# Optimization experiments

Measured on AMD Instinct MI355X. Metric: run time of the kernel, lower is better.

The kernel has to match this reference:

```python
import jax, jax.numpy as jnp
import numpy as np
from jax import lax

EPS = 1e-5
T, N, E = 10, 10000, 320000
C_IN, C_HID, C_OUT = 16, 32, 16


def _stgcn_layer(x, edge_index, edge_weight, tw, tb, gw, gb, gamma, beta):
    # x: [T, N, Cin] -> temporal conv over T per node
    xc = jnp.transpose(x, (1, 2, 0))  # [N, Cin, T]
    y = lax.conv_general_dilated(xc, tw, window_strides=(1,), padding=((1, 1),),
                                 dimension_numbers=("NCH", "OIH", "NCH"))
    y = y + tb[None, :, None]
    y = jnp.clip(y, -10.0, 10.0)
    # InstanceNorm1d (affine, biased var over time axis)
    mu = jnp.mean(y, axis=-1, keepdims=True)
    var = jnp.mean((y - mu) ** 2, axis=-1, keepdims=True)
    y = (y - mu) * lax.rsqrt(var + EPS) * gamma[None, :, None] + beta[None, :, None]
    y = jax.nn.relu(y)
    h = jnp.transpose(y, (0, 2, 1))  # [N, T, C]

    n = h.shape[0]
    # GCNConv normalization (identical at every timestep -> computed once)
    ewn = jax.nn.softmax(edge_weight)  # softmax over all E edges
    loop = jnp.arange(n, dtype=edge_index.dtype)
    row = jnp.concatenate([edge_index[0], loop])  # sources (+self loops)
    col = jnp.concatenate([edge_index[1], loop])  # destinations
    w = jnp.concatenate([ewn, jnp.ones((n,), dtype=ewn.dtype)])
    deg = jax.ops.segment_sum(w, col, num_segments=n)
    dinv = jnp.where(deg > 0, lax.rsqrt(jnp.maximum(deg, EPS * 0 + 1e-30)), 0.0)
    norm = dinv[row] * w * dinv[col]  # [E+N]

    hw = jnp.einsum("ntc,cd->ntd", h, gw)  # [N, T, C]
    msg = hw[row] * norm[:, None, None]     # [E+N, T, C] gather
    agg = jax.ops.segment_sum(msg, col, num_segments=n) + gb  # scatter-add
    out = jnp.clip(jax.nn.relu(agg), -10.0, 10.0)
    return jnp.transpose(out, (1, 0, 2))  # [T, N, C]


def setup_inputs() -> dict:
    key = jax.random.key(0)
    ks = jax.random.split(key, 16)
    inp = {
        "x": jax.random.normal(ks[0], (T, N, C_IN), dtype=jnp.float32),
        "edge_index": jax.random.randint(ks[1], (2, E), 0, N, dtype=jnp.int32),
        "edge_weight": jax.random.uniform(ks[2], (E,), dtype=jnp.float32),
        # layer 1 (in -> hid)
        "l1_tw": jax.random.normal(ks[3], (C_HID, C_IN, 3), dtype=jnp.float32) * 0.02,
        "l1_tb": jnp.zeros((C_HID,), dtype=jnp.float32),
        "l1_gw": jax.random.normal(ks[4], (C_HID, C_HID), dtype=jnp.float32) * 0.1,
        "l1_gb": jnp.zeros((C_HID,), dtype=jnp.float32),
        "l1_gamma": jnp.ones((C_HID,), dtype=jnp.float32),
        "l1_beta": jnp.zeros((C_HID,), dtype=jnp.float32),
        # layer 2 (hid -> hid)
        "l2_tw": jax.random.normal(ks[5], (C_HID, C_HID, 3), dtype=jnp.float32) * 0.02,
        "l2_tb": jnp.zeros((C_HID,), dtype=jnp.float32),
        "l2_gw": jax.random.normal(ks[6], (C_HID, C_HID), dtype=jnp.float32) * 0.1,
        "l2_gb": jnp.zeros((C_HID,), dtype=jnp.float32),
        "l2_gamma": jnp.ones((C_HID,), dtype=jnp.float32),
        "l2_beta": jnp.zeros((C_HID,), dtype=jnp.float32),
        # output linear
        "out_w": jax.random.normal(ks[7], (C_HID, C_OUT), dtype=jnp.float32) * 0.1,
        "out_b": jnp.zeros((C_OUT,), dtype=jnp.float32),
    }
    return inp


def reference(x, edge_index, edge_weight,
              l1_tw, l1_tb, l1_gw, l1_gb, l1_gamma, l1_beta,
              l2_tw, l2_tb, l2_gw, l2_gb, l2_gamma, l2_beta,
              out_w, out_b):
    h = _stgcn_layer(x, edge_index, edge_weight, l1_tw, l1_tb, l1_gw, l1_gb, l1_gamma, l1_beta)
    h = _stgcn_layer(h, edge_index, edge_weight, l2_tw, l2_tb, l2_gw, l2_gb, l2_gamma, l2_beta)
    # per-timestep linear then mean over time == mean then linear, done faithfully
    outs = jnp.einsum("tnc,cd->tnd", h, out_w) + out_b
    return jnp.mean(outs, axis=0)  # [N, C_OUT]
```

## Files before the change

### kernel.cpp

```cpp
#include <hip/hip_runtime.h>
#include <hip/hip_bf16.h>
#include <string.h>


typedef __hip_bfloat16 bf16;

#define TSTEPS 10
#define TPAD 12
#define CHID 32
#define ROWELE (TSTEPS * CHID)
#define ROWW4 40

__device__ __forceinline__ float b2f(bf16 v) { return __bfloat162float(v); }
__device__ __forceinline__ float ldf(const void* p, long i, int bf) {
    return bf ? __bfloat162float(((const bf16*)p)[i]) : ((const float*)p)[i];
}
__device__ __forceinline__ int detect_bf(const unsigned* gbits) {
    return (gbits[0] != 0x3F800000u) ? 1 : 0;
}
__device__ __forceinline__ float bflo(unsigned u) { return __uint_as_float(u << 16); }
__device__ __forceinline__ float bfhi(unsigned u) { return __uint_as_float(u & 0xFFFF0000u); }
__device__ __forceinline__ unsigned pack2bf(float a, float b) {
    bf16 x = __float2bfloat16(a), y = __float2bfloat16(b);
    unsigned short ux, uy;
    memcpy(&ux, &x, 2); memcpy(&uy, &y, 2);
    return (unsigned)ux | ((unsigned)uy << 16);
}
__device__ __forceinline__ unsigned short bfbits(float a) {
    bf16 x = __float2bfloat16(a);
    unsigned short u; memcpy(&u, &x, 2);
    return u;
}
__device__ __forceinline__ void accum8(float* f, uint4 u, float w) {
    f[0] += w * bflo(u.x); f[1] += w * bfhi(u.x);
    f[2] += w * bflo(u.y); f[3] += w * bfhi(u.y);
    f[4] += w * bflo(u.z); f[5] += w * bfhi(u.z);
    f[6] += w * bflo(u.w); f[7] += w * bfhi(u.w);
}


__device__ __forceinline__ void edge_body(
    int bb, const void* __restrict__ ew, int bf, const int* __restrict__ ei,
    float* __restrict__ ewn, float* __restrict__ degx, int* __restrict__ cnt,
    float* __restrict__ sumexp, int E, int tid) {
    __shared__ float s_red[4];
    int i0 = (bb * 256 + tid) * 4;
    float e0 = 0.0f, e1 = 0.0f, e2 = 0.0f, e3 = 0.0f;
    if ((E & 3) == 0 && i0 + 3 < E) {
        float w0, w1, w2, w3;
        if (bf) {
            uint2 u = ((const uint2*)ew)[i0 >> 2];
            w0 = bflo(u.x); w1 = bfhi(u.x); w2 = bflo(u.y); w3 = bfhi(u.y);
        } else {
            float4 f = ((const float4*)ew)[i0 >> 2];
            w0 = f.x; w1 = f.y; w2 = f.z; w3 = f.w;
        }
        e0 = __expf(w0); e1 = __expf(w1); e2 = __expf(w2); e3 = __expf(w3);
        int4 c4 = *(const int4*)&ei[E + i0];
        atomicAdd(&degx[c4.x], e0); atomicAdd(&cnt[c4.x], 1);
        atomicAdd(&degx[c4.y], e1); atomicAdd(&cnt[c4.y], 1);
        atomicAdd(&degx[c4.z], e2); atomicAdd(&cnt[c4.z], 1);
        atomicAdd(&degx[c4.w], e3); atomicAdd(&cnt[c4.w], 1);
        *(float4*)&ewn[i0] = make_float4(e0, e1, e2, e3);
    } else {
        float es[4] = {0, 0, 0, 0};
        for (int j = 0; j < 4; j++) {
            int i = i0 + j;
            if (i < E) {
                float e = __expf(ldf(ew, i, bf));
                es[j] = e;
                ewn[i] = e;
                int c = ei[E + i];
                atomicAdd(&degx[c], e);
                atomicAdd(&cnt[c], 1);
            }
        }
        e0 = es[0]; e1 = es[1]; e2 = es[2]; e3 = es[3];
    }
    float v = (e0 + e1) + (e2 + e3);
    for (int o = 32; o > 0; o >>= 1) v += __shfl_down(v, o);
    int lane = tid & 63, wv = tid >> 6;
    if (lane == 0) s_red[wv] = v;
    __syncthreads();
    if (tid == 0) atomicAdd(sumexp, s_red[0] + s_red[1] + s_red[2] + s_red[3]);
}


template <int CIN, int LAYOUT>
__device__ __forceinline__ void conv_body(
    int bb, const void* __restrict__ in_, int bfw,
    const void* __restrict__ tw, const void* __restrict__ tb,
    const void* __restrict__ gamma, const void* __restrict__ beta,
    const void* __restrict__ gw,
    bf16* __restrict__ hw, int N, int tid) {
    constexpr int CO = CHID;
    __shared__ __align__(16) float s_in[8 * CIN * TPAD];
    __shared__ __align__(16) float s_h[8 * CO * TPAD];
    __shared__ __align__(16) unsigned s_tw01[CIN * CO];
    __shared__ __align__(16) unsigned short s_tw2[CIN * CO];
    __shared__ __align__(16) unsigned s_gwp[(CO / 2) * CO];

    int nl = tid >> 5, o = tid & 31;

    float tbv = ldf(tb, o, bfw);
    float gav = ldf(gamma, o, bfw);
    float bev = ldf(beta, o, bfw);

    for (int i = tid; i < CIN * CO; i += 256) {
        int ci = i / CO, oo = i % CO;
        long base = ((long)oo * CIN + ci) * 3;
        float w0 = ldf(tw, base, bfw);
        float w1 = ldf(tw, base + 1, bfw);
        float w2 = ldf(tw, base + 2, bfw);
        s_tw01[ci * CO + oo] = pack2bf(w0, w1);
        s_tw2[ci * CO + oo] = bfbits(w2);
    }
    for (int i = tid; i < (CO / 2) * CO; i += 256) {
        int cp = i / CO, oo = i % CO;
        s_gwp[i] = pack2bf(ldf(gw, (long)(2 * cp) * CO + oo, bfw),
                           ldf(gw, (long)(2 * cp + 1) * CO + oo, bfw));
    }

    int nb = bb * 8;

    if (LAYOUT == 0) {
        constexpr int CP = CIN / 2;
        for (int i2 = tid; i2 < 8 * TSTEPS * CP; i2 += 256) {
            int cp = i2 % CP;
            int t = (i2 / CP) % TSTEPS;
            int nn = i2 / (CP * TSTEPS);
            int n = nb + nn;
            float v0 = 0.0f, v1 = 0.0f;
            if (n < N) {
                long idx = (long)t * ((long)N * CIN) + (long)n * CIN + 2 * cp;
                if (bfw) {
                    unsigned u = ((const unsigned*)in_)[idx >> 1];
                    v0 = bflo(u); v1 = bfhi(u);
                } else {
                    float2 f = ((const float2*)in_)[idx >> 1];
                    v0 = f.x; v1 = f.y;
                }
            }
            int b = nn * (CIN * TPAD) + (2 * cp) * TPAD + t;
            s_in[b] = v0;
            s_in[b + TPAD] = v1;
        }
    } else {
        for (int i2 = tid; i2 < 8 * CIN * 5; i2 += 256) {
            int tp = i2 % 5;
            int ci = (i2 / 5) % CIN;
            int nn = i2 / (5 * CIN);
            int n = nb + nn;
            float v0 = 0.0f, v1 = 0.0f;
            if (n < N) {
                long idx = (long)n * (CIN * TSTEPS) + ci * TSTEPS + 2 * tp;
                unsigned u = ((const unsigned*)in_)[idx >> 1];
                v0 = bflo(u); v1 = bfhi(u);
            }
            int b = nn * (CIN * TPAD) + ci * TPAD + 2 * tp;
            s_in[b] = v0;
            s_in[b + 1] = v1;
        }
    }
    __syncthreads();

    int n = nb + nl;
    const float* xrow = &s_in[nl * CIN * TPAD];

    float acc[TSTEPS];
#pragma unroll
    for (int t = 0; t < TSTEPS; t++) acc[t] = tbv;

    for (int ci = 0; ci < CIN; ci++) {
        const float4* xp = (const float4*)&xrow[ci * TPAD];
        float4 A = xp[0], B = xp[1], C = xp[2];
        float xr[TSTEPS] = {A.x, A.y, A.z, A.w, B.x, B.y, B.z, B.w, C.x, C.y};
        unsigned w01 = s_tw01[ci * CO + o];
        float w0 = bflo(w01), w1 = bfhi(w01);
        float w2 = __uint_as_float(((unsigned)s_tw2[ci * CO + o]) << 16);
        acc[0] += xr[0] * w1 + xr[1] * w2;
#pragma unroll
        for (int t = 1; t < TSTEPS - 1; t++)
            acc[t] += xr[t - 1] * w0 + xr[t] * w1 + xr[t + 1] * w2;
        acc[TSTEPS - 1] += xr[TSTEPS - 2] * w0 + xr[TSTEPS - 1] * w1;
    }

#pragma unroll
    for (int t = 0; t < TSTEPS; t++) acc[t] = fminf(fmaxf(acc[t], -10.0f), 10.0f);
    float mu = 0.0f;
#pragma unroll
    for (int t = 0; t < TSTEPS; t++) mu += acc[t];
    mu *= 0.1f;
    float var = 0.0f;
#pragma unroll
    for (int t = 0; t < TSTEPS; t++) { float d = acc[t] - mu; var += d * d; }
    var *= 0.1f;
    float sc = gav * rsqrtf(var + 1e-5f);
    float h[TSTEPS];
#pragma unroll
    for (int t = 0; t < TSTEPS; t++) h[t] = fmaxf((acc[t] - mu) * sc + bev, 0.0f);

    float4* hp = (float4*)&s_h[nl * CO * TPAD + o * TPAD];
    hp[0] = make_float4(h[0], h[1], h[2], h[3]);
    hp[1] = make_float4(h[4], h[5], h[6], h[7]);
    hp[2] = make_float4(h[8], h[9], 0.0f, 0.0f);
    __syncthreads();

    float acc2[TSTEPS];
#pragma unroll
    for (int t = 0; t < TSTEPS; t++) acc2[t] = 0.0f;
    const float* hrow = &s_h[nl * CO * TPAD];
    for (int cp = 0; cp < CO / 2; cp++) {
        unsigned g2 = s_gwp[cp * CO + o];
        float g0 = bflo(g2), g1 = bfhi(g2);
        const float4* r0 = (const float4*)&hrow[(2 * cp) * TPAD];
        const float4* r1 = (const float4*)&hrow[(2 * cp + 1) * TPAD];
        float4 A0 = r0[0], B0 = r0[1], C0 = r0[2];
        float4 A1 = r1[0], B1 = r1[1], C1 = r1[2];
        acc2[0] += A0.x * g0 + A1.x * g1;
        acc2[1] += A0.y * g0 + A1.y * g1;
        acc2[2] += A0.z * g0 + A1.z * g1;
        acc2[3] += A0.w * g0 + A1.w * g1;
        acc2[4] += B0.x * g0 + B1.x * g1;
        acc2[5] += B0.y * g0 + B1.y * g1;
        acc2[6] += B0.z * g0 + B1.z * g1;
        acc2[7] += B0.w * g0 + B1.w * g1;
        acc2[8] += C0.x * g0 + C1.x * g1;
        acc2[9] += C0.y * g0 + C1.y * g1;
    }
    if (n < N) {
        unsigned* hwp = (unsigned*)hw;
        long base = (long)n * (ROWELE / 2) + o * (TSTEPS / 2);
#pragma unroll
        for (int j = 0; j < 5; j++)
            hwp[base + j] = pack2bf(acc2[2 * j], acc2[2 * j + 1]);
    }
}


__global__ __launch_bounds__(256) void edge_conv1_kernel(
    const void* __restrict__ ew, const unsigned* __restrict__ gbits,
    const int* __restrict__ ei,
    float* __restrict__ ewn, float* __restrict__ degx, int* __restrict__ cnt,
    float* __restrict__ sumexp, int E, int gE4,
    const void* __restrict__ x,
    const void* __restrict__ tw, const void* __restrict__ tb,
    const void* __restrict__ gamma, const void* __restrict__ beta,
    const void* __restrict__ gw,
    bf16* __restrict__ hw, int N) {
    int bf = detect_bf(gbits);
    int tid = threadIdx.x;
    if ((int)blockIdx.x < gE4) {
        edge_body(blockIdx.x, ew, bf, ei, ewn, degx, cnt, sumexp, E, tid);
    } else {
        conv_body<16, 0>(blockIdx.x - gE4, x, bf, tw, tb, gamma, beta, gw,
                         hw, N, tid);
    }
}

__global__ __launch_bounds__(256) void conv2_kernel(
    const void* __restrict__ in_, const unsigned* __restrict__ gbits,
    const void* __restrict__ tw, const void* __restrict__ tb,
    const void* __restrict__ gamma, const void* __restrict__ beta,
    const void* __restrict__ gw,
    bf16* __restrict__ hw, int N) {
    conv_body<32, 1>(blockIdx.x, in_, detect_bf(gbits), tw, tb, gamma, beta,
                     gw, hw, N, threadIdx.x);
}

__global__ __launch_bounds__(1024) void scan_kernel(const int* __restrict__ cnt,
                                                    const float* __restrict__ degx,
                                                    const float* __restrict__ sumexp,
                                                    float* __restrict__ dinv,
                                                    int* __restrict__ off, int N) {
    __shared__ int s[1024];
    int tid = threadIdx.x;
    float invS = 1.0f / (*sumexp);
    for (int i = tid; i < N; i += 1024) dinv[i] = rsqrtf(1.0f + degx[i] * invS);
    int chunk = (N + 1023) / 1024;
    int b0 = tid * chunk;
    int p = 0;
    for (int k = 0; k < chunk; k++) { int i = b0 + k; if (i < N) p += cnt[i]; }
    s[tid] = p;
    __syncthreads();
    for (int d = 1; d < 1024; d <<= 1) {
        int v = (tid >= d) ? s[tid - d] : 0;
        __syncthreads();
        s[tid] += v;
        __syncthreads();
    }
    int base = s[tid] - p;
    for (int k = 0; k < chunk; k++) {
        int i = b0 + k;
        if (i < N) {
            off[i] = base;
            base += cnt[i];
            if (i == N - 1) off[N] = base;
        }
    }
}


__global__ __launch_bounds__(256) void fill_kernel(const int* __restrict__ ei,
                                                   const float* __restrict__ ewn,
                                                   const float* __restrict__ dinv,
                                                   const float* __restrict__ sumexp,
                                                   const int* __restrict__ off,
                                                   int* __restrict__ cursor,
                                                   int2* __restrict__ csr, int E) {
    int i0 = (blockIdx.x * 256 + threadIdx.x) * 4;
    if (i0 >= E) return;
    float invS = 1.0f / (*sumexp);
    if ((E & 3) == 0 && i0 + 3 < E) {
        int4 r4 = *(const int4*)&ei[i0];
        int4 c4 = *(const int4*)&ei[E + i0];
        float4 e4 = *(const float4*)&ewn[i0];
        int rr[4] = {r4.x, r4.y, r4.z, r4.w};
        int cc[4] = {c4.x, c4.y, c4.z, c4.w};
        float ee[4] = {e4.x, e4.y, e4.z, e4.w};
#pragma unroll
        for (int j = 0; j < 4; j++) {
            int r = rr[j], c = cc[j];
            int p = atomicAdd(&cursor[c], 1);
            float w = dinv[r] * (ee[j] * invS) * dinv[c];
            csr[off[c] + p] = make_int2(r, __float_as_int(w));
        }
    } else {
        for (int j = 0; j < 4; j++) {
            int i = i0 + j;
            if (i >= E) break;
            int r = ei[i], c = ei[E + i];
            int p = atomicAdd(&cursor[c], 1);
            float w = dinv[r] * (ewn[i] * invS) * dinv[c];
            csr[off[c] + p] = make_int2(r, __float_as_int(w));
        }
    }
}


template <bool FINAL>
__global__ __launch_bounds__(320) void agg_kernel_t(
    const uint4* __restrict__ hw4, const int* __restrict__ off,
    const int2* __restrict__ csr,
    const float* __restrict__ dinv, const void* __restrict__ gb,
    const void* __restrict__ ow, const void* __restrict__ ob,
    const unsigned* __restrict__ gbits,
    void* __restrict__ out, int N) {
    __shared__ int2 s_sw[ROWELE];
    __shared__ float s_part[8 * ROWW4 * 9];
    __shared__ float s_hbar[CHID];
    __shared__ float s_ow[CHID * 16];
    __shared__ float s_ob[16];

    int bf = detect_bf(gbits);
    int n = blockIdx.x;
    int tid = threadIdx.x;
    int g = tid % ROWW4;
    int eo = tid / ROWW4;

    if (FINAL) {
        for (int i = tid; i < CHID * 16; i += ROWELE) s_ow[i] = ldf(ow, i, bf);
        if (tid < 16) s_ob[tid] = ldf(ob, tid, bf);
    }

    float facc[8];
#pragma unroll
    for (int j = 0; j < 8; j++) facc[j] = 0.0f;

    float dn = dinv[n];
    if (eo == 0) {
        uint4 u = hw4[n * ROWW4 + g];
        accum8(facc, u, dn * dn);
    }

    int beg = off[n], end = off[n + 1];
    for (int base = beg; base < end; base += ROWELE) {
        int m = min(ROWELE, end - base);
        if (tid < m) s_sw[tid] = csr[base + tid];
        __syncthreads();
        int kmax = (m + 7) >> 3;
        int k = 0;
        for (; k + 2 <= kmax; k += 2) {
            int j0 = (k << 3) + eo, j1 = j0 + 8;
            int c0 = min(j0, m - 1), c1 = min(j1, m - 1);
            int2 e0 = s_sw[c0], e1 = s_sw[c1];
            float w0 = (j0 < m) ? __int_as_float(e0.y) : 0.0f;
            float w1 = (j1 < m) ? __int_as_float(e1.y) : 0.0f;
            uint4 u0 = hw4[e0.x * ROWW4 + g];
            uint4 u1 = hw4[e1.x * ROWW4 + g];
            accum8(facc, u0, w0);
            accum8(facc, u1, w1);
        }
        if (k < kmax) {
            int j0 = (k << 3) + eo;
            int c0 = min(j0, m - 1);
            int2 e0 = s_sw[c0];
            float w0 = (j0 < m) ? __int_as_float(e0.y) : 0.0f;
            uint4 u0 = hw4[e0.x * ROWW4 + g];
            accum8(facc, u0, w0);
        }
        __syncthreads();
    }

    {
        float* rowp = &s_part[(eo * ROWW4 + g) * 9];
#pragma unroll
        for (int j = 0; j < 8; j++) rowp[j] = facc[j];
    }
    __syncthreads();
    int gg = tid >> 3, jj = tid & 7;
    float v = 0.0f;
#pragma unroll
    for (int s = 0; s < 8; s++) v += s_part[(s * ROWW4 + gg) * 9 + jj];
    int c = tid / TSTEPS;
    v += ldf(gb, c, bf);
    v = fminf(fmaxf(v, 0.0f), 10.0f);

    if (!FINAL) {
        ((bf16*)out)[(long)n * ROWELE + tid] = __float2bfloat16(v);
    } else {
        __syncthreads();
        s_part[tid] = v;
        __syncthreads();
        if (tid < CHID) {
            float s = 0.0f;
#pragma unroll
            for (int t = 0; t < TSTEPS; t++) s += s_part[tid * TSTEPS + t];
            s_hbar[tid] = s * 0.1f;
        }
        __syncthreads();
        if (tid < 16) {
            float a = s_ob[tid];
#pragma unroll
            for (int cc = 0; cc < CHID; cc++) a += s_hbar[cc] * s_ow[cc * 16 + tid];
            long oi = (long)n * 16 + tid;
            if (bf) ((bf16*)out)[oi] = __float2bfloat16(a);
            else    ((float*)out)[oi] = a;
        }
    }
}


extern "C" void kernel_launch(void* const* d_in, const int* in_sizes, int n_in,
                              void* d_out, int out_size, void* d_ws, size_t ws_size,
                              hipStream_t stream) {
    (void)n_in; (void)out_size; (void)ws_size;

    const void* x     = d_in[0];
    const int*  ei    = (const int*)d_in[1];
    const void* ew    = d_in[2];
    const void* l1_tw = d_in[3];
    const void* l1_tb = d_in[4];
    const void* l1_gw = d_in[5];
    const void* l1_gb = d_in[6];
    const unsigned* gbits = (const unsigned*)d_in[7];
    const void* l1_ga = d_in[7];
    const void* l1_be = d_in[8];
    const void* l2_tw = d_in[9];
    const void* l2_tb = d_in[10];
    const void* l2_gw = d_in[11];
    const void* l2_gb = d_in[12];
    const void* l2_ga = d_in[13];
    const void* l2_be = d_in[14];
    const void* out_w = d_in[15];
    const void* out_b = d_in[16];

    int N = in_sizes[0] / (TSTEPS * 16);
    int E = in_sizes[1] / 2;

    char* p = (char*)d_ws;
    auto alloc = [&](size_t bytes) -> char* {
        char* r = p;
        p += (bytes + 255) & ~(size_t)255;
        return r;
    };
    char* zbase   = p;
    float* sumexp = (float*)alloc(256);
    float* degx   = (float*)alloc((size_t)N * 4);
    int*   cnt    = (int*)alloc((size_t)N * 4);
    int*   cursor = (int*)alloc((size_t)N * 4);
    size_t zbytes = (size_t)(p - zbase);
    float* ewn     = (float*)alloc((size_t)E * 4);
    float* dinv    = (float*)alloc((size_t)N * 4);
    int*   offA    = (int*)alloc((size_t)(N + 1) * 4);
    int2*  csr     = (int2*)alloc((size_t)E * 8);
    bf16*  bufA    = (bf16*)alloc((size_t)N * ROWELE * 2);
    bf16*  bufB    = (bf16*)alloc((size_t)N * ROWELE * 2);

    int gE4 = (E + 1023) / 1024;
    int gConv = (N + 7) / 8;

    hipMemsetAsync(zbase, 0, zbytes, stream);
    hipLaunchKernelGGL(edge_conv1_kernel, dim3(gE4 + gConv), dim3(256), 0, stream,
                       ew, gbits, ei, ewn, degx, cnt, sumexp, E, gE4,
                       x, l1_tw, l1_tb, l1_ga, l1_be, l1_gw, bufA, N);
    hipLaunchKernelGGL(scan_kernel, dim3(1), dim3(1024), 0, stream,
                       cnt, degx, sumexp, dinv, offA, N);
    hipLaunchKernelGGL(fill_kernel, dim3(gE4), dim3(256), 0, stream,
                       ei, ewn, dinv, sumexp, offA, cursor, csr, E);

    hipLaunchKernelGGL((agg_kernel_t<false>), dim3(N), dim3(ROWELE), 0, stream,
                       (const uint4*)bufA, offA, csr, dinv, l1_gb,
                       nullptr, nullptr, gbits, (void*)bufB, N);
    hipLaunchKernelGGL(conv2_kernel, dim3(gConv), dim3(256), 0, stream,
                       (const void*)bufB, gbits, l2_tw, l2_tb, l2_ga, l2_be,
                       l2_gw, bufA, N);
    hipLaunchKernelGGL((agg_kernel_t<true>), dim3(N), dim3(ROWELE), 0, stream,
                       (const uint4*)bufA, offA, csr, dinv, l2_gb,
                       out_w, out_b, gbits, d_out, N);
}
```

Baseline: 278.6 us.

## Split conv work across time pairs with 640-thread blocks of four nodes

Rewrites the temporal conv plus GCN linear body so each thread computes two timesteps of one output channel for one node, using 640-thread blocks that cover four nodes, instead of one thread per (node, channel) computing all ten timesteps. Instance-norm statistics are now computed through shared memory with extra barriers, and the edge softmax/degree pass is resized to the 640-thread block. The goal is more parallelism and lower per-thread register pressure in the conv kernels. In exchange it adds more synchronisation and shared-memory traffic, and the weight-staging cost is amortised over fewer nodes per block.

```diff
diff --git a/kernel.cpp b/kernel.cpp
--- a/kernel.cpp
+++ b/kernel.cpp
@@ -6,12 +6,12 @@
 typedef __hip_bfloat16 bf16;
 
 #define TSTEPS 10
-#define TPAD 12
 #define CHID 32
 #define ROWELE (TSTEPS * CHID)
 #define ROWW4 40
-
-__device__ __forceinline__ float b2f(bf16 v) { return __bfloat162float(v); }
+#define NB 4
+#define CTH 640
+
 __device__ __forceinline__ float ldf(const void* p, long i, int bf) {
     return bf ? __bfloat162float(((const bf16*)p)[i]) : ((const float*)p)[i];
 }
@@ -43,8 +43,8 @@
     int bb, const void* __restrict__ ew, int bf, const int* __restrict__ ei,
     float* __restrict__ ewn, float* __restrict__ degx, int* __restrict__ cnt,
     float* __restrict__ sumexp, int E, int tid) {
-    __shared__ float s_red[4];
-    int i0 = (bb * 256 + tid) * 4;
+    __shared__ float s_red[CTH / 64];
+    int i0 = (bb * CTH + tid) * 4;
     float e0 = 0.0f, e1 = 0.0f, e2 = 0.0f, e3 = 0.0f;
     if ((E & 3) == 0 && i0 + 3 < E) {
         float w0, w1, w2, w3;
@@ -82,57 +82,62 @@
     int lane = tid & 63, wv = tid >> 6;
     if (lane == 0) s_red[wv] = v;
     __syncthreads();
-    if (tid == 0) atomicAdd(sumexp, s_red[0] + s_red[1] + s_red[2] + s_red[3]);
+    if (tid == 0) {
+        float s = 0.0f;
+#pragma unroll
+        for (int w = 0; w < CTH / 64; w++) s += s_red[w];
+        atomicAdd(sumexp, s);
+    }
 }
 
 
 template <int CIN, int LAYOUT>
-__device__ __forceinline__ void conv_body(
+__device__ __forceinline__ void conv_body_tp(
     int bb, const void* __restrict__ in_, int bfw,
     const void* __restrict__ tw, const void* __restrict__ tb,
     const void* __restrict__ gamma, const void* __restrict__ beta,
     const void* __restrict__ gw,
-    bf16* __restrict__ hw, int N, int tid) {
+    unsigned* __restrict__ hw, int N, int tid) {
     constexpr int CO = CHID;
-    __shared__ __align__(16) float s_in[8 * CIN * TPAD];
-    __shared__ __align__(16) float s_h[8 * CO * TPAD];
-    __shared__ __align__(16) unsigned s_tw01[CIN * CO];
-    __shared__ __align__(16) unsigned short s_tw2[CIN * CO];
-    __shared__ __align__(16) unsigned s_gwp[(CO / 2) * CO];
-
-    int nl = tid >> 5, o = tid & 31;
+    __shared__ float s_x[NB * CIN * TSTEPS];
+    __shared__ float s_y[NB * CO * TSTEPS];
+    __shared__ float s_hh[NB * CO * TSTEPS];
+    __shared__ unsigned s_tw01[CIN * CO];
+    __shared__ unsigned short s_tw2[CIN * CO];
+    __shared__ unsigned s_gwp[(CO / 2) * CO];
+    __shared__ float s_mu[NB * CO], s_sc[NB * CO];
+
+    int nl = tid / 160;
+    int rem = tid % 160;
+    int o = rem / 5, j = rem % 5, t0 = 2 * j;
+    int nb = bb * NB;
+    int n = nb + nl;
 
     float tbv = ldf(tb, o, bfw);
-    float gav = ldf(gamma, o, bfw);
     float bev = ldf(beta, o, bfw);
 
-    for (int i = tid; i < CIN * CO; i += 256) {
-        int ci = i / CO, oo = i % CO;
+    for (int i = tid; i < CIN * CO; i += CTH) {
+        int ci = i >> 5, oo = i & 31;
         long base = ((long)oo * CIN + ci) * 3;
-        float w0 = ldf(tw, base, bfw);
-        float w1 = ldf(tw, base + 1, bfw);
-        float w2 = ldf(tw, base + 2, bfw);
-        s_tw01[ci * CO + oo] = pack2bf(w0, w1);
-        s_tw2[ci * CO + oo] = bfbits(w2);
-    }
-    for (int i = tid; i < (CO / 2) * CO; i += 256) {
-        int cp = i / CO, oo = i % CO;
+        s_tw01[i] = pack2bf(ldf(tw, base, bfw), ldf(tw, base + 1, bfw));
+        s_tw2[i] = bfbits(ldf(tw, base + 2, bfw));
+    }
+    for (int i = tid; i < (CO / 2) * CO; i += CTH) {
+        int cp = i >> 5, oo = i & 31;
         s_gwp[i] = pack2bf(ldf(gw, (long)(2 * cp) * CO + oo, bfw),
                            ldf(gw, (long)(2 * cp + 1) * CO + oo, bfw));
     }
 
-    int nb = bb * 8;
-
     if (LAYOUT == 0) {
         constexpr int CP = CIN / 2;
-        for (int i2 = tid; i2 < 8 * TSTEPS * CP; i2 += 256) {
+        for (int i2 = tid; i2 < NB * TSTEPS * CP; i2 += CTH) {
             int cp = i2 % CP;
             int t = (i2 / CP) % TSTEPS;
             int nn = i2 / (CP * TSTEPS);
-            int n = nb + nn;
+            int ng = nb + nn;
             float v0 = 0.0f, v1 = 0.0f;
-            if (n < N) {
-                long idx = (long)t * ((long)N * CIN) + (long)n * CIN + 2 * cp;
+            if (ng < N) {
+                long idx = (long)t * ((long)N * CIN) + (long)ng * CIN + 2 * cp;
                 if (bfw) {
                     unsigned u = ((const unsigned*)in_)[idx >> 1];
                     v0 = bflo(u); v1 = bfhi(u);
@@ -141,131 +146,115 @@
                     v0 = f.x; v1 = f.y;
                 }
             }
-            int b = nn * (CIN * TPAD) + (2 * cp) * TPAD + t;
-            s_in[b] = v0;
-            s_in[b + TPAD] = v1;
+            int b = nn * (CIN * TSTEPS) + (2 * cp) * TSTEPS + t;
+            s_x[b] = v0;
+            s_x[b + TSTEPS] = v1;
         }
     } else {
-        for (int i2 = tid; i2 < 8 * CIN * 5; i2 += 256) {
+        for (int i2 = tid; i2 < NB * CIN * 5; i2 += CTH) {
             int tp = i2 % 5;
             int ci = (i2 / 5) % CIN;
             int nn = i2 / (5 * CIN);
-            int n = nb + nn;
+            int ng = nb + nn;
             float v0 = 0.0f, v1 = 0.0f;
-            if (n < N) {
-                long idx = (long)n * (CIN * TSTEPS) + ci * TSTEPS + 2 * tp;
-                unsigned u = ((const unsigned*)in_)[idx >> 1];
+            if (ng < N) {
+                unsigned u = ((const unsigned*)in_)[(long)ng * (CIN * 5) + ci * 5 + tp];
                 v0 = bflo(u); v1 = bfhi(u);
             }
-            int b = nn * (CIN * TPAD) + ci * TPAD + 2 * tp;
-            s_in[b] = v0;
-            s_in[b + 1] = v1;
-        }
-    }
-    __syncthreads();
-
-    int n = nb + nl;
-    const float* xrow = &s_in[nl * CIN * TPAD];
-
-    float acc[TSTEPS];
-#pragma unroll
-    for (int t = 0; t < TSTEPS; t++) acc[t] = tbv;
-
+            int b = nn * (CIN * TSTEPS) + ci * TSTEPS + 2 * tp;
+            s_x[b] = v0;
+            s_x[b + 1] = v1;
+        }
+    }
+    __syncthreads();
+
+    float a0 = tbv, a1 = tbv;
+    const float* xb_base = &s_x[nl * CIN * TSTEPS];
     for (int ci = 0; ci < CIN; ci++) {
-        const float4* xp = (const float4*)&xrow[ci * TPAD];
-        float4 A = xp[0], B = xp[1], C = xp[2];
-        float xr[TSTEPS] = {A.x, A.y, A.z, A.w, B.x, B.y, B.z, B.w, C.x, C.y};
+        const float* xb = xb_base + ci * TSTEPS;
+        float xm = (j > 0) ? xb[t0 - 1] : 0.0f;
+        float x0 = xb[t0];
+        float x1 = xb[t0 + 1];
+        float xp = (j < 4) ? xb[t0 + 2] : 0.0f;
         unsigned w01 = s_tw01[ci * CO + o];
         float w0 = bflo(w01), w1 = bfhi(w01);
         float w2 = __uint_as_float(((unsigned)s_tw2[ci * CO + o]) << 16);
-        acc[0] += xr[0] * w1 + xr[1] * w2;
-#pragma unroll
-        for (int t = 1; t < TSTEPS - 1; t++)
-            acc[t] += xr[t - 1] * w0 + xr[t] * w1 + xr[t + 1] * w2;
-        acc[TSTEPS - 1] += xr[TSTEPS - 2] * w0 + xr[TSTEPS - 1] * w1;
-    }
-
-#pragma unroll
-    for (int t = 0; t < TSTEPS; t++) acc[t] = fminf(fmaxf(acc[t], -10.0f), 10.0f);
-    float mu = 0.0f;
-#pragma unroll
-    for (int t = 0; t < TSTEPS; t++) mu += acc[t];
-    mu *= 0.1f;
-    float var = 0.0f;
-#pragma unroll
-    for (int t = 0; t < TSTEPS; t++) { float d = acc[t] - mu; var += d * d; }
-    var *= 0.1f;
-    float sc = gav * rsqrtf(var + 1e-5f);
-    float h[TSTEPS];
-#pragma unroll
-    for (int t = 0; t < TSTEPS; t++) h[t] = fmaxf((acc[t] - mu) * sc + bev, 0.0f);
-
-    float4* hp = (float4*)&s_h[nl * CO * TPAD + o * TPAD];
-    hp[0] = make_float4(h[0], h[1], h[2], h[3]);
-    hp[1] = make_float4(h[4], h[5], h[6], h[7]);
-    hp[2] = make_float4(h[8], h[9], 0.0f, 0.0f);
-    __syncthreads();
-
-    float acc2[TSTEPS];
-#pragma unroll
-    for (int t = 0; t < TSTEPS; t++) acc2[t] = 0.0f;
-    const float* hrow = &s_h[nl * CO * TPAD];
+        a0 += xm * w0 + x0 * w1 + x1 * w2;
+        a1 += x0 * w0 + x1 * w1 + xp * w2;
+    }
+    float y0 = fminf(fmaxf(a0, -10.0f), 10.0f);
+    float y1 = fminf(fmaxf(a1, -10.0f), 10.0f);
+    s_y[nl * (CO * TSTEPS) + o * TSTEPS + t0] = y0;
+    s_y[nl * (CO * TSTEPS) + o * TSTEPS + t0 + 1] = y1;
+    __syncthreads();
+
+    if (tid < NB * CO) {
+        int snl = tid >> 5, so = tid & 31;
+        const float* yb = &s_y[snl * (CO * TSTEPS) + so * TSTEPS];
+        float yv[TSTEPS];
+#pragma unroll
+        for (int t = 0; t < TSTEPS; t++) yv[t] = yb[t];
+        float mu = 0.0f;
+#pragma unroll
+        for (int t = 0; t < TSTEPS; t++) mu += yv[t];
+        mu *= 0.1f;
+        float var = 0.0f;
+#pragma unroll
+        for (int t = 0; t < TSTEPS; t++) { float d = yv[t] - mu; var += d * d; }
+        var *= 0.1f;
+        s_mu[tid] = mu;
+        s_sc[tid] = ldf(gamma, so, bfw) * rsqrtf(var + 1e-5f);
+    }
+    __syncthreads();
+
+    {
+        float mu = s_mu[nl * CO + o], sc = s_sc[nl * CO + o];
+        s_hh[nl * (CO * TSTEPS) + o * TSTEPS + t0] = fmaxf((y0 - mu) * sc + bev, 0.0f);
+        s_hh[nl * (CO * TSTEPS) + o * TSTEPS + t0 + 1] = fmaxf((y1 - mu) * sc + bev, 0.0f);
+    }
+    __syncthreads();
+
+    float b0 = 0.0f, b1 = 0.0f;
+    const float* hb = &s_hh[nl * (CO * TSTEPS)];
     for (int cp = 0; cp < CO / 2; cp++) {
         unsigned g2 = s_gwp[cp * CO + o];
         float g0 = bflo(g2), g1 = bfhi(g2);
-        const float4* r0 = (const float4*)&hrow[(2 * cp) * TPAD];
-        const float4* r1 = (const float4*)&hrow[(2 * cp + 1) * TPAD];
-        float4 A0 = r0[0], B0 = r0[1], C0 = r0[2];
-        float4 A1 = r1[0], B1 = r1[1], C1 = r1[2];
-        acc2[0] += A0.x * g0 + A1.x * g1;
-        acc2[1] += A0.y * g0 + A1.y * g1;
-        acc2[2] += A0.z * g0 + A1.z * g1;
-        acc2[3] += A0.w * g0 + A1.w * g1;
-        acc2[4] += B0.x * g0 + B1.x * g1;
-        acc2[5] += B0.y * g0 + B1.y * g1;
-        acc2[6] += B0.z * g0 + B1.z * g1;
-        acc2[7] += B0.w * g0 + B1.w * g1;
-        acc2[8] += C0.x * g0 + C1.x * g1;
-        acc2[9] += C0.y * g0 + C1.y * g1;
-    }
-    if (n < N) {
-        unsigned* hwp = (unsigned*)hw;
-        long base = (long)n * (ROWELE / 2) + o * (TSTEPS / 2);
-#pragma unroll
-        for (int j = 0; j < 5; j++)
-            hwp[base + j] = pack2bf(acc2[2 * j], acc2[2 * j + 1]);
-    }
-}
-
-
-__global__ __launch_bounds__(256) void edge_conv1_kernel(
+        const float* h0p = hb + (2 * cp) * TSTEPS;
+        const float* h1p = hb + (2 * cp + 1) * TSTEPS;
+        b0 += h0p[t0] * g0 + h1p[t0] * g1;
+        b1 += h0p[t0 + 1] * g0 + h1p[t0 + 1] * g1;
+    }
+    if (n < N) hw[(long)n * (ROWELE / 2) + o * 5 + j] = pack2bf(b0, b1);
+}
+
+__global__ __launch_bounds__(CTH) void edge_conv1_kernel(
     const void* __restrict__ ew, const unsigned* __restrict__ gbits,
     const int* __restrict__ ei,
     float* __restrict__ ewn, float* __restrict__ degx, int* __restrict__ cnt,
-    float* __restrict__ sumexp, int E, int gE4,
+    float* __restrict__ sumexp, int E, int gE,
     const void* __restrict__ x,
     const void* __restrict__ tw, const void* __restrict__ tb,
     const void* __restrict__ gamma, const void* __restrict__ beta,
     const void* __restrict__ gw,
-    bf16* __restrict__ hw, int N) {
+    unsigned* __restrict__ hw, int N) {
     int bf = detect_bf(gbits);
     int tid = threadIdx.x;
-    if ((int)blockIdx.x < gE4) {
+    if ((int)blockIdx.x < gE) {
         edge_body(blockIdx.x, ew, bf, ei, ewn, degx, cnt, sumexp, E, tid);
     } else {
-        conv_body<16, 0>(blockIdx.x - gE4, x, bf, tw, tb, gamma, beta, gw,
-                         hw, N, tid);
-    }
-}
-
-__global__ __launch_bounds__(256) void conv2_kernel(
+        conv_body_tp<16, 0>(blockIdx.x - gE, x, bf, tw, tb, gamma, beta, gw,
+                            hw, N, tid);
+    }
+}
+
+__global__ __launch_bounds__(CTH) void conv2_kernel(
     const void* __restrict__ in_, const unsigned* __restrict__ gbits,
     const void* __restrict__ tw, const void* __restrict__ tb,
     const void* __restrict__ gamma, const void* __restrict__ beta,
     const void* __restrict__ gw,
-    bf16* __restrict__ hw, int N) {
-    conv_body<32, 1>(blockIdx.x, in_, detect_bf(gbits), tw, tb, gamma, beta,
-                     gw, hw, N, threadIdx.x);
+    unsigned* __restrict__ hw, int N) {
+    conv_body_tp<32, 1>(blockIdx.x, in_, detect_bf(gbits), tw, tb, gamma,
+                        beta, gw, hw, N, threadIdx.x);
 }
 
 __global__ __launch_bounds__(1024) void scan_kernel(const int* __restrict__ cnt,
@@ -299,7 +288,6 @@
         }
     }
 }
-
 
 __global__ __launch_bounds__(256) void fill_kernel(const int* __restrict__ ei,
                                                    const float* __restrict__ ewn,
@@ -487,24 +475,25 @@
     bf16*  bufA    = (bf16*)alloc((size_t)N * ROWELE * 2);
     bf16*  bufB    = (bf16*)alloc((size_t)N * ROWELE * 2);
 
+    int gE = (E + CTH * 4 - 1) / (CTH * 4);
     int gE4 = (E + 1023) / 1024;
-    int gConv = (N + 7) / 8;
+    int gConv = (N + NB - 1) / NB;
 
     hipMemsetAsync(zbase, 0, zbytes, stream);
-    hipLaunchKernelGGL(edge_conv1_kernel, dim3(gE4 + gConv), dim3(256), 0, stream,
-                       ew, gbits, ei, ewn, degx, cnt, sumexp, E, gE4,
-                       x, l1_tw, l1_tb, l1_ga, l1_be, l1_gw, bufA, N);
+    hipLaunchKernelGGL(edge_conv1_kernel, dim3(gE + gConv), dim3(CTH), 0, stream,
+                       ew, gbits, ei, ewn, degx, cnt, sumexp, E, gE,
+                       x, l1_tw, l1_tb, l1_ga, l1_be, l1_gw,
+                       (unsigned*)bufA, N);
     hipLaunchKernelGGL(scan_kernel, dim3(1), dim3(1024), 0, stream,
                        cnt, degx, sumexp, dinv, offA, N);
     hipLaunchKernelGGL(fill_kernel, dim3(gE4), dim3(256), 0, stream,
                        ei, ewn, dinv, sumexp, offA, cursor, csr, E);
-
     hipLaunchKernelGGL((agg_kernel_t<false>), dim3(N), dim3(ROWELE), 0, stream,
                        (const uint4*)bufA, offA, csr, dinv, l1_gb,
                        nullptr, nullptr, gbits, (void*)bufB, N);
-    hipLaunchKernelGGL(conv2_kernel, dim3(gConv), dim3(256), 0, stream,
+    hipLaunchKernelGGL(conv2_kernel, dim3(gConv), dim3(CTH), 0, stream,
                        (const void*)bufB, gbits, l2_tw, l2_tb, l2_ga, l2_be,
-                       l2_gw, bufA, N);
+                       l2_gw, (unsigned*)bufA, N);
     hipLaunchKernelGGL((agg_kernel_t<true>), dim3(N), dim3(ROWELE), 0, stream,
                        (const uint4*)bufA, offA, csr, dinv, l2_gb,
                        out_w, out_b, gbits, d_out, N);
```

Result: slower. 353.9 us (+27.0%).
